# Performance work log

Hardware: AMD Instinct MI355X
Metric: run time of the kernel (lower is better)

## Reference

```python
import jax, jax.numpy as jnp
import numpy as np

SIZE_U = 1000
SIZE_V = 1000
D = 128          # input_dim
NW = 2           # num_weights
NC = 2           # num_classes
M_EXTRA = 16     # extra rows beyond size_u+size_v (the 'M' slice)


def setup_inputs() -> dict:
    key = jax.random.key(0)
    k1, k2, k3 = jax.random.split(key, 3)
    feature = jax.random.normal(k1, (SIZE_U + SIZE_V + M_EXTRA, D), dtype=jnp.float32)
    # kaiming-uniform-like scale for the bilinear weights and classifier
    weight = jax.random.uniform(k2, (NW, D, D), dtype=jnp.float32,
                                minval=-1.0, maxval=1.0) * float(np.sqrt(6.0 / D))
    weight_classifier = jax.random.uniform(k3, (NW, NC), dtype=jnp.float32,
                                           minval=-1.0, maxval=1.0) * float(np.sqrt(6.0 / NW))
    return {"feature": feature, "weight": weight, "weight_classifier": weight_classifier}


def reference(feature, weight, weight_classifier):
    # dropout treated as identity (inference mode)
    lnc = feature[:SIZE_U]                       # [U, D]
    dis = feature[SIZE_U:SIZE_U + SIZE_V]        # [V, D]
    M = feature[SIZE_U + SIZE_V:]                # [M_EXTRA, D]

    # Per-weight bilinear score: scores[u,v,k] = lnc[u] @ W_k @ dis[v]
    # Reordered (project-then-score) to avoid the O(U*V*D^2) naive expansion,
    # but math is identical to the original pairwise loop.
    proj = jnp.einsum('kde,ud->kue', weight, lnc)          # [NW, U, D]
    scores = jnp.einsum('kue,ve->uvk', proj, dis)          # [U, V, NW]
    scores = scores.reshape(SIZE_U * SIZE_V, NW)           # matches meshgrid('ij') flatten order

    outputs = jax.nn.relu(scores @ weight_classifier)      # [U*V, NC]

    # Replicated pair features, as returned by the original module
    lnc_rep = jnp.repeat(lnc, SIZE_V, axis=0)              # [U*V, D] (row_idx varies slowest)
    dis_rep = jnp.tile(dis, (SIZE_U, 1))                   # [U*V, D]
    return (outputs, lnc_rep, dis_rep, M)
```

## Files before the change

kernel.cpp:

```cpp
#include <hip/hip_runtime.h>

#define SIZE_U 1000
#define SIZE_V 1000
#define DIM    128
#define M_EXTRA 16

#define OUT_LNC_OFF 2000000L
#define OUT_DIS_OFF 130000000L
#define OUT_M_OFF   258000000L

__global__ __launch_bounds__(256) void bilinear_split_kernel(
    const float* __restrict__ feature,
    const float* __restrict__ weight,
    const float* __restrict__ wc,
    float* __restrict__ out)
{
    const int b = blockIdx.x;
    const int t = threadIdx.x;

    if (b == 2 * SIZE_U) {
        const float4* src = (const float4*)(feature + (size_t)(SIZE_U + SIZE_V) * DIM);
        float4* dst = (float4*)(out + OUT_M_OFF);
        for (int i = t; i < (M_EXTRA * DIM) / 4; i += 256) dst[i] = src[i];
        return;
    }

    const int u  = b >> 1;
    const int c  = t & 31;
    const int rg = t >> 5;
    const float4* dis4 = (const float4*)(feature + (size_t)SIZE_U * DIM);
    const size_t rowbase = (size_t)u * SIZE_V;

    if ((b & 1) == 0) {
        const float4 lnc4 = ((const float4*)(feature + (size_t)u * DIM))[c];
        float4* lr = (float4*)(out + OUT_LNC_OFF) + rowbase * (DIM / 4);
        float4* dr = (float4*)(out + OUT_DIS_OFF) + rowbase * (DIM / 4);
        #pragma unroll 4
        for (int r = rg; r < SIZE_V; r += 8) {
            const int idx = r * 32 + c;
            const float4 dv = dis4[idx];
            lr[idx] = lnc4;
            dr[idx] = dv;
        }
    } else {
        __shared__ float lnc_s[DIM];
        __shared__ float proj_s[2][DIM];
        __shared__ float q_s[2][DIM];

        if (t < DIM) lnc_s[t] = feature[(size_t)u * DIM + t];
        __syncthreads();

        {
            const int k = t >> 7, e = t & 127;
            const float* wk = weight + (size_t)k * DIM * DIM + e;
            float acc = 0.f;
            #pragma unroll 8
            for (int d = 0; d < DIM; ++d)
                acc = fmaf(wk[(size_t)d * DIM], lnc_s[d], acc);
            proj_s[k][e] = acc;
        }
        __syncthreads();

        {
            const int cc = t >> 7, e = t & 127;
            q_s[cc][e] = wc[cc] * proj_s[0][e] + wc[2 + cc] * proj_s[1][e];
        }
        __syncthreads();

        const float4 q0 = ((const float4*)q_s[0])[c];
        const float4 q1 = ((const float4*)q_s[1])[c];
        float2* outp = (float2*)out;

        for (int r = rg; r < SIZE_V; r += 8) {
            const float4 dv = dis4[r * 32 + c];
            float t0 = dv.x * q0.x + dv.y * q0.y + dv.z * q0.z + dv.w * q0.w;
            float t1 = dv.x * q1.x + dv.y * q1.y + dv.z * q1.z + dv.w * q1.w;
            #pragma unroll
            for (int off = 16; off; off >>= 1) {
                t0 += __shfl_xor(t0, off);
                t1 += __shfl_xor(t1, off);
            }
            if (c == 0)
                outp[rowbase + r] = make_float2(t0 > 0.f ? t0 : 0.f,
                                                t1 > 0.f ? t1 : 0.f);
        }
    }
}

extern "C" void kernel_launch(void* const* d_in, const int* in_sizes, int n_in,
                              void* d_out, int out_size, void* d_ws, size_t ws_size,
                              hipStream_t stream) {
    const float* feature = (const float*)d_in[0];
    const float* weight  = (const float*)d_in[1];
    const float* wc      = (const float*)d_in[2];
    float* out = (float*)d_out;

    bilinear_split_kernel<<<2 * SIZE_U + 1, 256, 0, stream>>>(feature, weight, wc, out);
}
```

Before: 209.0 us.

## Split rows per block in half, regroup block roles, use nontemporal stores

Each u-row of work is split across two blocks covering 500 rows each, which doubles the grid. Blocks are interleaved in groups of 8 so that copy blocks and score blocks alternate in contiguous chunks. The replicated lnc/dis output writes now use nontemporal stores, which should cut cache pollution on the roughly 1 GB write stream. The cost is that each score block recomputes the 128x128 projection twice as often.

```diff
diff --git a/kernel.cpp b/kernel.cpp
--- a/kernel.cpp
+++ b/kernel.cpp
@@ -5,11 +5,13 @@
 #define DIM    128
 #define M_EXTRA 16
 
+typedef float f32x4 __attribute__((ext_vector_type(4)));
+
 #define OUT_LNC_OFF 2000000L
 #define OUT_DIS_OFF 130000000L
 #define OUT_M_OFF   258000000L
 
-__global__ __launch_bounds__(256) void bilinear_split_kernel(
+__global__ __launch_bounds__(256) void bilinear_v3_kernel(
     const float* __restrict__ feature,
     const float* __restrict__ weight,
     const float* __restrict__ wc,
@@ -18,29 +20,35 @@
     const int b = blockIdx.x;
     const int t = threadIdx.x;
 
-    if (b == 2 * SIZE_U) {
-        const float4* src = (const float4*)(feature + (size_t)(SIZE_U + SIZE_V) * DIM);
-        float4* dst = (float4*)(out + OUT_M_OFF);
+    if (b == 4000) {
+        const f32x4* src = (const f32x4*)(feature + (size_t)(SIZE_U + SIZE_V) * DIM);
+        f32x4* dst = (f32x4*)(out + OUT_M_OFF);
         for (int i = t; i < (M_EXTRA * DIM) / 4; i += 256) dst[i] = src[i];
         return;
     }
 
-    const int u  = b >> 1;
+    const int g    = b >> 3;
+    const int role = g & 1;
+    const int j    = (g >> 1) * 8 + (b & 7);
+    const int u    = j >> 1;
+    const int r0   = (j & 1) * 500;
+    const int r1   = r0 + 500;
+
     const int c  = t & 31;
     const int rg = t >> 5;
-    const float4* dis4 = (const float4*)(feature + (size_t)SIZE_U * DIM);
+    const f32x4* dis4 = (const f32x4*)(feature + (size_t)SIZE_U * DIM);
     const size_t rowbase = (size_t)u * SIZE_V;
 
-    if ((b & 1) == 0) {
-        const float4 lnc4 = ((const float4*)(feature + (size_t)u * DIM))[c];
-        float4* lr = (float4*)(out + OUT_LNC_OFF) + rowbase * (DIM / 4);
-        float4* dr = (float4*)(out + OUT_DIS_OFF) + rowbase * (DIM / 4);
+    if (role == 0) {
+        const f32x4 lnc4 = ((const f32x4*)(feature + (size_t)u * DIM))[c];
+        f32x4* lr = (f32x4*)(out + OUT_LNC_OFF) + rowbase * (DIM / 4);
+        f32x4* dr = (f32x4*)(out + OUT_DIS_OFF) + rowbase * (DIM / 4);
         #pragma unroll 4
-        for (int r = rg; r < SIZE_V; r += 8) {
+        for (int r = r0 + rg; r < r1; r += 8) {
             const int idx = r * 32 + c;
-            const float4 dv = dis4[idx];
-            lr[idx] = lnc4;
-            dr[idx] = dv;
+            const f32x4 dv = dis4[idx];
+            __builtin_nontemporal_store(lnc4, &lr[idx]);
+            __builtin_nontemporal_store(dv, &dr[idx]);
         }
     } else {
         __shared__ float lnc_s[DIM];
@@ -67,12 +75,12 @@
         }
         __syncthreads();
 
-        const float4 q0 = ((const float4*)q_s[0])[c];
-        const float4 q1 = ((const float4*)q_s[1])[c];
+        const f32x4 q0 = ((const f32x4*)q_s[0])[c];
+        const f32x4 q1 = ((const f32x4*)q_s[1])[c];
         float2* outp = (float2*)out;
 
-        for (int r = rg; r < SIZE_V; r += 8) {
-            const float4 dv = dis4[r * 32 + c];
+        for (int r = r0 + rg; r < r1; r += 8) {
+            const f32x4 dv = dis4[r * 32 + c];
             float t0 = dv.x * q0.x + dv.y * q0.y + dv.z * q0.z + dv.w * q0.w;
             float t1 = dv.x * q1.x + dv.y * q1.y + dv.z * q1.z + dv.w * q1.w;
             #pragma unroll
@@ -95,5 +103,5 @@
     const float* wc      = (const float*)d_in[2];
     float* out = (float*)d_out;
 
-    bilinear_split_kernel<<<2 * SIZE_U + 1, 256, 0, stream>>>(feature, weight, wc, out);
+    bilinear_v3_kernel<<<4001, 256, 0, stream>>>(feature, weight, wc, out);
 }
```

After: 203.2 us. 2.7% less time.
